# Optimization experiments

Hardware: AMD Instinct MI355X
Metric: run time of the kernel (lower is better)

The kernel has to match this reference:

```python
import jax, jax.numpy as jnp
import numpy as np
import math

NUM_HEADS = 16
KEY_SIZE = 64
HIDDEN = 4096
EMBED = 1024
VOCAB = 32000
SEQ = 2048
LAYERS = 4


def rmsnorm(x):
    return x * jax.lax.rsqrt(jnp.mean(x * x, axis=-1, keepdims=True) + 1e-5)


def rope_buffers(seq, d):
    half = d // 2
    i = jnp.arange(d)
    offset = i % half
    scales = jnp.power(10000.0, (-2.0 / d) * offset.astype(jnp.float32))
    m = jnp.arange(seq, dtype=jnp.float32)
    angles = m[:, None] * scales[None, :]  # [S, D]
    cos = jnp.cos(angles)
    sin = jnp.sin(angles)
    sin = jnp.concatenate([-sin[:, :half], sin[:, half:]], axis=-1)
    return cos, sin


def rotate(x, cos, sin):
    # x: [B, H, S, D]; cos/sin: [S, D]
    half = KEY_SIZE // 2
    swapped = jnp.concatenate([x[..., half:], x[..., :half]], axis=-1)
    return cos[None, None] * x + sin[None, None] * swapped


def setup_inputs() -> dict:
    key = jax.random.key(0)
    ks = jax.random.split(key, 7)
    std = 0.02
    return {
        'tokens': jax.random.randint(ks[0], (1, SEQ), 0, VOCAB),
        'table': jax.random.normal(ks[1], (VOCAB, EMBED), jnp.float32) * std,
        'qkv_w': jax.random.normal(ks[2], (LAYERS, EMBED, 3 * NUM_HEADS * KEY_SIZE), jnp.float32) * std,
        'out_w': jax.random.normal(ks[3], (LAYERS, NUM_HEADS * KEY_SIZE, EMBED), jnp.float32) * std,
        'up_w': jax.random.normal(ks[4], (LAYERS, EMBED, 2 * HIDDEN), jnp.float32) * std,
        'down_w': jax.random.normal(ks[5], (LAYERS, HIDDEN, EMBED), jnp.float32) * std,
        'vocab_w': jax.random.normal(ks[6], (EMBED, VOCAB), jnp.float32) * std,
    }


def reference(tokens, table, qkv_w, out_w, up_w, down_w, vocab_w):
    B, S = tokens.shape
    H, D = NUM_HEADS, KEY_SIZE
    # module zeroes embedding row 0 each forward
    table = table.at[0].set(0.0)
    cos, sin = rope_buffers(S, D)
    causal = jnp.tril(jnp.ones((S, S), dtype=bool))  # context_size == S -> pure causal
    emb = table[tokens]  # [B, S, E]
    for l in range(LAYERS):
        # --- self attention ---
        normed = rmsnorm(emb)
        qkv = normed @ qkv_w[l]  # [B, S, 3HD]
        q, k, v = jnp.split(qkv, 3, axis=-1)
        q = q.reshape(B, S, H, D).transpose(0, 2, 1, 3)
        k = k.reshape(B, S, H, D).transpose(0, 2, 1, 3)
        v = v.reshape(B, S, H, D).transpose(0, 2, 1, 3)
        q = rotate(q, cos, sin)
        k = rotate(k, cos, sin)
        attn = jnp.einsum('bhqd,bhkd->bhqk', q, k) / math.sqrt(D)
        attn = jnp.where(causal[None, None], attn, -jnp.inf)
        attn = jax.nn.softmax(attn, axis=-1)
        out = jnp.einsum('bhqk,bhkd->bhqd', attn, v)
        out = out.transpose(0, 2, 1, 3).reshape(B, S, H * D)
        emb = emb + out @ out_w[l]
        # --- SwiGLU FFN ---
        normed = rmsnorm(emb)
        gate_up = normed @ up_w[l]
        gate, up = gate_up[..., :HIDDEN], gate_up[..., HIDDEN:]
        emb = emb + (up * jax.nn.silu(gate)) @ down_w[l]
    emb = rmsnorm(emb)
    logits = emb @ vocab_w  # [B, S, V]
    return logits
```

## Files before the change

kernel.cpp:

```cpp
#include <hip/hip_runtime.h>
#include <hip/hip_bf16.h>

typedef __attribute__((ext_vector_type(8))) short short8;
typedef __attribute__((ext_vector_type(4))) float f32x4;

__device__ __forceinline__ ushort f2bf(float f) {
  uint32_t u = __float_as_uint(f);
  uint32_t r = (u + 0x7FFFu + ((u >> 16) & 1u)) >> 16;
  return (ushort)r;
}
__device__ __forceinline__ float bf2f(ushort u) {
  return __uint_as_float(((uint32_t)u) << 16);
}

__device__ __forceinline__ void gload_lds16(const ushort* g, ushort* l) {
  __builtin_amdgcn_global_load_lds(
      (const __attribute__((address_space(1))) void*)g,
      (__attribute__((address_space(3))) void*)l, 16, 0, 0);
}

__device__ __forceinline__ f32x4 mfma16(short8 a, short8 b, f32x4 c) {
  return __builtin_amdgcn_mfma_f32_16x16x32_bf16(a, b, c, 0, 0, 0);
}

#define BAR() __builtin_amdgcn_s_barrier()
#define WAIT_LGKM()                                        \
  do {                                                     \
    asm volatile("s_waitcnt lgkmcnt(0)" ::: "memory");     \
    __builtin_amdgcn_sched_barrier(0);                     \
  } while (0)
#define WAIT_VM0()                                         \
  do {                                                     \
    asm volatile("s_waitcnt vmcnt(0)" ::: "memory");       \
    __builtin_amdgcn_sched_barrier(0);                     \
  } while (0)
#define WAIT_VM4()                                         \
  do {                                                     \
    asm volatile("s_waitcnt vmcnt(4)" ::: "memory");       \
    __builtin_amdgcn_sched_barrier(0);                     \
  } while (0)

__global__ __launch_bounds__(256)
void transpose_conv_kernel(const float* __restrict__ W, ushort* __restrict__ WT,
                           const int K, const int N, const int mode) {
  const size_t lofs = (size_t)blockIdx.z * K * N;
  W += lofs;
  WT += lofs;
  __shared__ float tile[64][65];
  const int n0 = blockIdx.x * 64;
  const int k0 = blockIdx.y * 64;
  const int t = threadIdx.x;
#pragma unroll
  for (int j = 0; j < 4; ++j) {
    const int idx = j * 1024 + t * 4;
    const int kk = idx >> 6, nn = idx & 63;
    *(float4*)&tile[kk][nn] = *(const float4*)&W[(size_t)(k0 + kk) * N + n0 + nn];
  }
  __syncthreads();
#pragma unroll
  for (int j = 0; j < 4; ++j) {
    const int idx = j * 1024 + t * 4;
    const int nn = idx >> 6, kk = idx & 63;
    int rr = n0 + nn;
    if (mode == 1) rr = (rr < 4096) ? (2 * rr) : (2 * (rr - 4096) + 1);
    ushort4 o;
    o.x = f2bf(tile[kk + 0][nn]);
    o.y = f2bf(tile[kk + 1][nn]);
    o.z = f2bf(tile[kk + 2][nn]);
    o.w = f2bf(tile[kk + 3][nn]);
    *(ushort4*)&WT[(size_t)rr * K + k0 + kk] = o;
  }
}

__global__ __launch_bounds__(256)
void sincos_kernel(float2* __restrict__ cstab) {
  const int idx = blockIdx.x * 256 + threadIdx.x;
  const int s = idx >> 5, o = idx & 31;
  const float freq = exp2f(-0.41524101186092029f * (float)o);
  const float a = (float)s * freq;
  cstab[idx] = make_float2(cosf(a), sinf(a));
}

__global__ __launch_bounds__(256)
void embed_norm_kernel(const int* __restrict__ tokens, const float* __restrict__ table,
                       float* __restrict__ emb, ushort* __restrict__ normed) {
  const int s = blockIdx.x, t = threadIdx.x;
  const int tok = tokens[s];
  float4 v = make_float4(0.f, 0.f, 0.f, 0.f);
  if (tok != 0) v = *(const float4*)&table[(size_t)tok * 1024 + t * 4];
  *(float4*)&emb[(size_t)s * 1024 + t * 4] = v;
  float ss = v.x * v.x + v.y * v.y + v.z * v.z + v.w * v.w;
#pragma unroll
  for (int off = 32; off; off >>= 1) ss += __shfl_xor(ss, off);
  __shared__ float red[4];
  if ((t & 63) == 0) red[t >> 6] = ss;
  __syncthreads();
  const float total = red[0] + red[1] + red[2] + red[3];
  const float sc = rsqrtf(total * (1.f / 1024.f) + 1e-5f);
  ushort4 o;
  o.x = f2bf(v.x * sc); o.y = f2bf(v.y * sc);
  o.z = f2bf(v.z * sc); o.w = f2bf(v.w * sc);
  *(ushort4*)&normed[(size_t)s * 1024 + t * 4] = o;
}

__global__ __launch_bounds__(256)
void rmsnorm_kernel(const float* __restrict__ x, ushort* __restrict__ out) {
  const int row = blockIdx.x, t = threadIdx.x;
  const float4 v = *(const float4*)&x[(size_t)row * 1024 + t * 4];
  float ss = v.x * v.x + v.y * v.y + v.z * v.z + v.w * v.w;
#pragma unroll
  for (int off = 32; off; off >>= 1) ss += __shfl_xor(ss, off);
  __shared__ float red[4];
  if ((t & 63) == 0) red[t >> 6] = ss;
  __syncthreads();
  const float total = red[0] + red[1] + red[2] + red[3];
  const float sc = rsqrtf(total * (1.f / 1024.f) + 1e-5f);
  ushort4 o;
  o.x = f2bf(v.x * sc); o.y = f2bf(v.y * sc);
  o.z = f2bf(v.z * sc); o.w = f2bf(v.w * sc);
  *(ushort4*)&out[(size_t)row * 1024 + t * 4] = o;
}

__global__ __launch_bounds__(512)
void attn_mfma_kernel(const ushort* __restrict__ qh, const ushort* __restrict__ kh,
                      const ushort* __restrict__ vt, float* __restrict__ wso,
                      float* __restrict__ wsml) {
  __shared__ ushort sQ[128 * 64];
  __shared__ ushort sK[2][64 * 64];
  __shared__ ushort sV[2][64 * 64];
  __shared__ ushort sP[8][1024];
  const int h = blockIdx.y;
  const int u = blockIdx.x;
  const int qt_raw = u >> 1, half = u & 1;
  const int qt = (h < 8) ? qt_raw : 15 - qt_raw;
  const int i0 = qt * 128;
  const int tid = threadIdx.x;
  const int w = tid >> 6, lane = tid & 63;
  const int llo = lane & 15, lhi = lane >> 4;
  const ushort* qg = qh + ((size_t)h * 2048 + i0) * 64;
  const ushort* kg = kh + (size_t)h * 2048 * 64;
  const ushort* vg = vt + (size_t)h * 64 * 2048;

  const int scb = w * 64;
  const int sch = scb + lane;
  const int srow = sch >> 3, sc = sch & 7;
  auto stage_kv = [&](int kb, int b) {
    gload_lds16(kg + (size_t)(kb + srow) * 64 + ((sc ^ (srow & 7)) * 8),
                &sK[b][scb * 8]);
    gload_lds16(vg + (size_t)srow * 2048 + kb + ((sc ^ (srow & 7)) * 8),
                &sV[b][scb * 8]);
  };

  const int c0 = half ? (qt + 1) : 0;
  const int c1 = half ? (2 * qt + 2) : (qt + 1);

#pragma unroll
  for (int j = 0; j < 2; ++j) {
    const int cb = j * 512 + w * 64;
    const int ch = cb + lane;
    const int row = ch >> 3, c = ch & 7;
    gload_lds16(qg + (size_t)row * 64 + ((c ^ (row & 7)) * 8), &sQ[cb * 8]);
  }
  stage_kv(c0 * 64, 0);
  __syncthreads();
  const int qrow = w * 16 + llo;
  const short8 qf0 = *(const short8*)&sQ[qrow * 64 + ((lhi ^ (qrow & 7)) * 8)];
  const short8 qf1 = *(const short8*)&sQ[qrow * 64 + (((4 + lhi) ^ (qrow & 7)) * 8)];
  const int wmax = i0 + w * 16 + 15;

  float m = -1e30f, lsum = 0.f;
  f32x4 o[4] = {};
  int bufc = 0;
  for (int cb2 = c0; cb2 < c1; ++cb2) {
    const int kb = cb2 * 64;
    if (cb2 + 1 < c1) stage_kv((cb2 + 1) * 64, bufc ^ 1);

    if (kb <= wmax) {
      f32x4 st[4] = {};
#pragma unroll
      for (int ck = 0; ck < 2; ++ck) {
        const short8 qf = ck ? qf1 : qf0;
#pragma unroll
        for (int f = 0; f < 4; ++f) {
          const int key = f * 16 + llo;
          const short8 kf = *(const short8*)&sK[bufc][key * 64 + (((ck * 4 + lhi) ^ (key & 7)) * 8)];
          st[f] = mfma16(kf, qf, st[f]);
        }
      }

      float pv[4][4];
      const bool edge = (kb + 63 > i0 + w * 16);
#pragma unroll
      for (int f = 0; f < 4; ++f)
#pragma unroll
        for (int r = 0; r < 4; ++r) {
          float x = st[f][r] * 0.125f;
          if (edge && (kb - i0 + f * 16 + lhi * 4 + r) > qrow) x = -1e30f;
          pv[f][r] = x;
        }
      float mr = pv[0][0];
#pragma unroll
      for (int f = 0; f < 4; ++f)
#pragma unroll
        for (int r = 0; r < 4; ++r) mr = fmaxf(mr, pv[f][r]);
      mr = fmaxf(mr, __shfl_xor(mr, 16));
      mr = fmaxf(mr, __shfl_xor(mr, 32));
      const float mnew = fmaxf(m, mr);
      const float scale = __expf(m - mnew);
      m = mnew;
      float rs = 0.f;
#pragma unroll
      for (int f = 0; f < 4; ++f)
#pragma unroll
        for (int r = 0; r < 4; ++r) {
          const float p = __expf(pv[f][r] - mnew);
          pv[f][r] = p;
          rs += p;
        }
      rs += __shfl_xor(rs, 16);
      rs += __shfl_xor(rs, 32);
      lsum = lsum * scale + rs;
      float scr[4];
#pragma unroll
      for (int r = 0; r < 4; ++r) scr[r] = __shfl(scale, lhi * 4 + r);
#pragma unroll
      for (int nn = 0; nn < 4; ++nn)
#pragma unroll
        for (int r = 0; r < 4; ++r) o[nn][r] *= scr[r];

      ushort* pw = sP[w];
#pragma unroll
      for (int f = 0; f < 4; ++f) {
        uint2 pk;
        pk.x = (uint)f2bf(pv[f][0]) | ((uint)f2bf(pv[f][1]) << 16);
        pk.y = (uint)f2bf(pv[f][2]) | ((uint)f2bf(pv[f][3]) << 16);
        *(uint2*)&pw[llo * 64 + ((f * 16 + lhi * 4) ^ ((llo & 7) << 3))] = pk;
      }
      const short8 pf0 = *(const short8*)&pw[llo * 64 + ((lhi ^ (llo & 7)) * 8)];
      const short8 pf1 = *(const short8*)&pw[llo * 64 + (((4 + lhi) ^ (llo & 7)) * 8)];

#pragma unroll
      for (int ck = 0; ck < 2; ++ck) {
        const short8 pf = ck ? pf1 : pf0;
#pragma unroll
        for (int nn = 0; nn < 4; ++nn) {
          const int drow = nn * 16 + llo;
          const short8 vf = *(const short8*)&sV[bufc][drow * 64 + (((ck * 4 + lhi) ^ (drow & 7)) * 8)];
          o[nn] = mfma16(pf, vf, o[nn]);
        }
      }
    }

    __syncthreads();
    bufc ^= 1;
  }

#pragma unroll
  for (int nn = 0; nn < 4; ++nn)
#pragma unroll
    for (int r = 0; r < 4; ++r) {
      const int row = i0 + w * 16 + lhi * 4 + r;
      wso[((size_t)(half * 16 + h) * 2048 + row) * 64 + nn * 16 + llo] = o[nn][r];
    }
  if (lhi == 0) {
    const int row = i0 + w * 16 + llo;
    *(float2*)&wsml[((size_t)(half * 16 + h) * 2048 + row) * 2] = make_float2(m, lsum);
  }
}

__global__ __launch_bounds__(256)
void attn_merge_kernel(const float* __restrict__ wso, const float* __restrict__ wsml,
                       ushort* __restrict__ attn_out) {
  const int row = blockIdx.x;
  const int t = threadIdx.x;
  const int h = t >> 4, dg = t & 15;
  const float2 ml1 = *(const float2*)&wsml[((size_t)h * 2048 + row) * 2];
  const float2 ml2 = *(const float2*)&wsml[((size_t)(16 + h) * 2048 + row) * 2];
  const float m = fmaxf(ml1.x, ml2.x);
  const float w1 = __expf(ml1.x - m), w2 = __expf(ml2.x - m);
  const float inv = 1.f / (ml1.y * w1 + ml2.y * w2);
  const float4 o1 = *(const float4*)&wso[((size_t)h * 2048 + row) * 64 + dg * 4];
  const float4 o2 = *(const float4*)&wso[((size_t)(16 + h) * 2048 + row) * 64 + dg * 4];
  ushort4 o;
  o.x = f2bf((o1.x * w1 + o2.x * w2) * inv);
  o.y = f2bf((o1.y * w1 + o2.y * w2) * inv);
  o.z = f2bf((o1.z * w1 + o2.z * w2) * inv);
  o.w = f2bf((o1.w * w1 + o2.w * w2) * inv);
  *(ushort4*)&attn_out[(size_t)row * 1024 + h * 64 + dg * 4] = o;
}

template <int BM, int BN, int EPI>
__global__ __launch_bounds__(256)
void gemm_bt64_kernel(const ushort* __restrict__ A, const ushort* __restrict__ BT,
                      const float* __restrict__ addend, void* __restrict__ Cout,
                      const int M, const int N, const int K) {
  constexpr int WM = BM / 2, WN = BN / 2;
  constexpr int FM = WM / 16, FN = WN / 16;
  __shared__ ushort sA[BM * 64];
  __shared__ ushort sB[BN * 64];
  const int bm0 = blockIdx.y * BM;
  const int bn0 = blockIdx.x * BN;
  const int tid = threadIdx.x;
  const int wid = tid >> 6, lane = tid & 63;
  const int wr = wid >> 1, wc = wid & 1;
  const int lhi = lane >> 4, llo = lane & 15;
  f32x4 acc[FM][FN] = {};
  for (int kt = 0; kt < K; kt += 64) {
#pragma unroll
    for (int i = 0; i < BM * 8 / 256; ++i) {
      const int cb = i * 256 + wid * 64;
      const int ch = cb + lane;
      const int row = ch >> 3, c = ch & 7;
      gload_lds16(A + (size_t)(bm0 + row) * K + kt + ((c ^ (row & 7)) * 8),
                  sA + (size_t)cb * 8);
    }
#pragma unroll
    for (int i = 0; i < BN * 8 / 256; ++i) {
      const int cb = i * 256 + wid * 64;
      const int ch = cb + lane;
      const int row = ch >> 3, c = ch & 7;
      gload_lds16(BT + (size_t)(bn0 + row) * K + kt + ((c ^ (row & 7)) * 8),
                  sB + (size_t)cb * 8);
    }
    __syncthreads();
    short8 aF[FM][2], bF[FN][2];
#pragma unroll
    for (int mm = 0; mm < FM; ++mm) {
      const int row = wr * WM + mm * 16 + llo;
#pragma unroll
      for (int ks = 0; ks < 2; ++ks)
        aF[mm][ks] = *(const short8*)&sA[row * 64 + (((ks * 4 + lhi) ^ (row & 7)) * 8)];
    }
#pragma unroll
    for (int nn = 0; nn < FN; ++nn) {
      const int row = wc * WN + nn * 16 + llo;
#pragma unroll
      for (int ks = 0; ks < 2; ++ks)
        bF[nn][ks] = *(const short8*)&sB[row * 64 + (((ks * 4 + lhi) ^ (row & 7)) * 8)];
    }
#pragma unroll
    for (int mm = 0; mm < FM; ++mm)
#pragma unroll
      for (int nn = 0; nn < FN; ++nn)
#pragma unroll
        for (int ks = 0; ks < 2; ++ks)
          acc[mm][nn] = mfma16(aF[mm][ks], bF[nn][ks], acc[mm][nn]);
    __syncthreads();
  }
#pragma unroll
  for (int mm = 0; mm < FM; ++mm) {
#pragma unroll
    for (int nn = 0; nn < FN; ++nn) {
      const int col = bn0 + wc * WN + nn * 16 + llo;
#pragma unroll
      for (int r = 0; r < 4; ++r) {
        const int row = bm0 + wr * WM + mm * 16 + lhi * 4 + r;
        float v = acc[mm][nn][r];
        if constexpr (EPI == 1) v += addend[(size_t)row * N + col];
        ((float*)Cout)[(size_t)row * N + col] = v;
      }
    }
  }
}

__global__ __launch_bounds__(256)
void gemm_qkv_kernel(const ushort* __restrict__ A, const ushort* __restrict__ BT,
                     const float2* __restrict__ cstab, ushort* __restrict__ qh,
                     ushort* __restrict__ kh, ushort* __restrict__ vt, const int K) {
  constexpr int BM = 128, BN = 128, WM = 64, WN = 64, FM = 4, FN = 4;
  __shared__ ushort sA[BM * 64];
  __shared__ ushort sB[BN * 64];
  const int bm0 = blockIdx.y * BM;
  const int bn0 = blockIdx.x * BN;
  const int tid = threadIdx.x;
  const int wid = tid >> 6, lane = tid & 63;
  const int wr = wid >> 1, wc = wid & 1;
  const int lhi = lane >> 4, llo = lane & 15;
  f32x4 acc[FM][FN] = {};
  for (int kt = 0; kt < K; kt += 64) {
#pragma unroll
    for (int i = 0; i < 4; ++i) {
      const int cb = i * 256 + wid * 64;
      const int ch = cb + lane;
      const int row = ch >> 3, c = ch & 7;
      gload_lds16(A + (size_t)(bm0 + row) * K + kt + ((c ^ (row & 7)) * 8),
                  sA + (size_t)cb * 8);
    }
#pragma unroll
    for (int i = 0; i < 4; ++i) {
      const int cb = i * 256 + wid * 64;
      const int ch = cb + lane;
      const int row = ch >> 3, c = ch & 7;
      gload_lds16(BT + (size_t)(bn0 + row) * K + kt + ((c ^ (row & 7)) * 8),
                  sB + (size_t)cb * 8);
    }
    __syncthreads();
    short8 aF[FM][2], bF[FN][2];
#pragma unroll
    for (int mm = 0; mm < FM; ++mm) {
      const int row = wr * WM + mm * 16 + llo;
#pragma unroll
      for (int ks = 0; ks < 2; ++ks)
        aF[mm][ks] = *(const short8*)&sA[row * 64 + (((ks * 4 + lhi) ^ (row & 7)) * 8)];
    }
#pragma unroll
    for (int nn = 0; nn < FN; ++nn) {
      const int row = wc * WN + nn * 16 + llo;
#pragma unroll
      for (int ks = 0; ks < 2; ++ks)
        bF[nn][ks] = *(const short8*)&sB[row * 64 + (((ks * 4 + lhi) ^ (row & 7)) * 8)];
    }
#pragma unroll
    for (int mm = 0; mm < FM; ++mm)
#pragma unroll
      for (int nn = 0; nn < FN; ++nn)
#pragma unroll
        for (int ks = 0; ks < 2; ++ks)
          acc[mm][nn] = mfma16(aF[mm][ks], bF[nn][ks], acc[mm][nn]);
    __syncthreads();
  }
#pragma unroll
  for (int mm = 0; mm < FM; ++mm) {
    const int row_base = bm0 + wr * WM + mm * 16 + lhi * 4;
#pragma unroll
    for (int nn = 0; nn < FN; ++nn) {
      const int col = bn0 + wc * WN + nn * 16 + llo;
      const int part = col >> 10;
      const int hcol = col & 1023;
      const int h = hcol >> 6;
      const int d = hcol & 63;
      const int off = d & 31;
      if (part == 2) {
        ushort4 o;
        o.x = f2bf(acc[mm][nn][0]);
        o.y = f2bf(acc[mm][nn][1]);
        o.z = f2bf(acc[mm][nn][2]);
        o.w = f2bf(acc[mm][nn][3]);
        *(ushort4*)&vt[((size_t)h * 64 + d) * 2048 + row_base] = o;
      } else {
#pragma unroll
        for (int r = 0; r < 4; ++r) {
          const int row = row_base + r;
          const float v = acc[mm][nn][r];
          const float pt = acc[mm][nn ^ 2][r];
          const float2 cn = cstab[row * 32 + off];
          const float si = (d < 32) ? -cn.y : cn.y;
          const ushort o = f2bf(cn.x * v + si * pt);
          const size_t ho = ((size_t)h * 2048 + row) * 64 + d;
          if (part == 0) qh[ho] = o; else kh[ho] = o;
        }
      }
    }
  }
}

template <int EPI>
__global__ __launch_bounds__(512, 2)
void gemm8p_kernel(const ushort* __restrict__ A, const ushort* __restrict__ BT,
                   void* __restrict__ Cout,
                   const int M, const int N, const int K, const int nby) {
  extern __shared__ ushort smem[];
  const int nwg = gridDim.x;
  const int cpx = nwg >> 3;
  int id = blockIdx.x;
  id = (id & 7) * cpx + (id >> 3);
  const int by = id % nby, bx = id / nby;
  const int bm0 = by * 256, bn0 = bx * 256;
  const int tid = threadIdx.x;
  const int wid = tid >> 6, lane = tid & 63;
  const int wr = wid >> 2, wc = wid & 3;
  const int llo = lane & 15, lhi = lane >> 4;
  const ushort* gA = A + (size_t)bm0 * K;
  const ushort* gB = BT + (size_t)bn0 * K;

  auto stage = [&](ushort* dst, int kt) {
#pragma unroll
    for (int i = 0; i < 2; ++i) {
      const int cb = i * 512 + wid * 64;
      const int ch = cb + lane;
      const int row = ch >> 2, c = ch & 3;
      gload_lds16(gA + (size_t)row * K + kt + ((c ^ ((row >> 1) & 3)) * 8),
                  dst + (size_t)cb * 8);
    }
#pragma unroll
    for (int i = 0; i < 2; ++i) {
      const int cb = i * 512 + wid * 64;
      const int ch = cb + lane;
      const int row = ch >> 2, c = ch & 3;
      gload_lds16(gB + (size_t)row * K + kt + ((c ^ ((row >> 1) & 3)) * 8),
                  dst + 8192 + (size_t)cb * 8);
    }
  };

  f32x4 acc[8][4] = {};
  short8 aF[4], bF[4];

  const int nt = K >> 5;
  stage(smem, 0);
  stage(smem + 16384, 32);
  WAIT_VM4();
  BAR();

  int cs = 0;
  for (int t = 0; t < nt; ++t) {
    ushort* cA = smem + cs * 16384;
    ushort* cB = cA + 8192;
    int ss = cs + 2; if (ss >= 3) ss -= 3;
    const bool pf2 = (t + 2 < nt);
    if (pf2) stage(smem + ss * 16384, (t + 2) * 32);
#pragma unroll
    for (int mm = 0; mm < 4; ++mm) {
      const int row = wr * 128 + mm * 16 + llo;
      aF[mm] = *(const short8*)&cA[row * 32 + ((lhi ^ ((row >> 1) & 3)) * 8)];
    }
#pragma unroll
    for (int nn = 0; nn < 4; ++nn) {
      const int row = wc * 64 + nn * 16 + llo;
      bF[nn] = *(const short8*)&cB[row * 32 + ((lhi ^ ((row >> 1) & 3)) * 8)];
    }
    BAR(); WAIT_LGKM();
    __builtin_amdgcn_s_setprio(1);
#pragma unroll
    for (int mm = 0; mm < 4; ++mm)
#pragma unroll
      for (int nn = 0; nn < 4; ++nn)
        acc[mm][nn] = mfma16(aF[mm], bF[nn], acc[mm][nn]);
    __builtin_amdgcn_s_setprio(0);
    BAR();
#pragma unroll
    for (int mm = 0; mm < 4; ++mm) {
      const int row = wr * 128 + (mm + 4) * 16 + llo;
      aF[mm] = *(const short8*)&cA[row * 32 + ((lhi ^ ((row >> 1) & 3)) * 8)];
    }
    BAR(); WAIT_LGKM();
    __builtin_amdgcn_s_setprio(1);
#pragma unroll
    for (int mm = 0; mm < 4; ++mm)
#pragma unroll
      for (int nn = 0; nn < 4; ++nn)
        acc[mm + 4][nn] = mfma16(aF[mm], bF[nn], acc[mm + 4][nn]);
    __builtin_amdgcn_s_setprio(0);
    if (pf2) { WAIT_VM4(); } else { WAIT_VM0(); }
    BAR();
    ++cs; if (cs == 3) cs = 0;
  }

#pragma unroll
  for (int m = 0; m < 8; ++m) {
#pragma unroll
    for (int n = 0; n < 4; ++n) {
      const int col = bn0 + wc * 64 + n * 16 + llo;
#pragma unroll
      for (int r = 0; r < 4; ++r) {
        const int row = bm0 + wr * 128 + m * 16 + lhi * 4 + r;
        float v = acc[m][n][r];
        if constexpr (EPI == 3) {
          const float other = __shfl_xor(v, 1);
          if ((llo & 1) == 0) {
            const float gate = v, up = other;
            const float hh = up * gate / (1.f + expf(-gate));
            ((ushort*)Cout)[(size_t)row * (N >> 1) + (col >> 1)] = f2bf(hh);
          }
        } else {
          ((float*)Cout)[(size_t)row * N + col] = v;
        }
      }
    }
  }
}

extern "C" void kernel_launch(void* const* d_in, const int* in_sizes, int n_in,
                              void* d_out, int out_size, void* d_ws, size_t ws_size,
                              hipStream_t stream) {
  const int* tokens    = (const int*)d_in[0];
  const float* table   = (const float*)d_in[1];
  const float* qkv_w   = (const float*)d_in[2];
  const float* out_w   = (const float*)d_in[3];
  const float* up_w    = (const float*)d_in[4];
  const float* down_w  = (const float*)d_in[5];
  const float* vocab_w = (const float*)d_in[6];
  float* logits = (float*)d_out;

  constexpr int G8P_LDS = 98304;
  hipFuncSetAttribute(reinterpret_cast<const void*>(&gemm8p_kernel<0>),
                      hipFuncAttributeMaxDynamicSharedMemorySize, G8P_LDS);
  hipFuncSetAttribute(reinterpret_cast<const void*>(&gemm8p_kernel<3>),
                      hipFuncAttributeMaxDynamicSharedMemorySize, G8P_LDS);

  char* p = (char*)d_ws;
  auto alloc = [&](size_t bytes) {
    char* r = p;
    p += (bytes + 255) & ~(size_t)255;
    return r;
  };
  float*  emb    = (float*)alloc(2048ull * 1024 * 4);
  ushort* normed = (ushort*)alloc(2048ull * 1024 * 2);
  float2* cstab  = (float2*)alloc(2048ull * 32 * 8);
  ushort* qhb    = (ushort*)alloc(16ull * 2048 * 64 * 2);
  ushort* khb    = (ushort*)alloc(16ull * 2048 * 64 * 2);
  ushort* vtb    = (ushort*)alloc(16ull * 64 * 2048 * 2);
  ushort* attno  = (ushort*)alloc(2048ull * 1024 * 2);
  float*  wso    = (float*)alloc(2ull * 16 * 2048 * 64 * 4);
  float*  wsml   = (float*)alloc(2ull * 16 * 2048 * 2 * 4);
  ushort* hbuf   = (ushort*)alloc(2048ull * 4096 * 2);
  ushort* qkvT   = (ushort*)alloc(4ull * 3072 * 1024 * 2);
  ushort* outT   = (ushort*)alloc(4ull * 1024 * 1024 * 2);
  ushort* upT    = (ushort*)alloc(4ull * 8192 * 1024 * 2);
  ushort* downT  = (ushort*)alloc(4ull * 1024 * 4096 * 2);
  ushort* vocabT = (ushort*)alloc(32000ull * 1024 * 2);

  transpose_conv_kernel<<<dim3(3072 / 64, 1024 / 64, 4), 256, 0, stream>>>(
      qkv_w, qkvT, 1024, 3072, 0);
  transpose_conv_kernel<<<dim3(1024 / 64, 1024 / 64, 4), 256, 0, stream>>>(
      out_w, outT, 1024, 1024, 0);
  transpose_conv_kernel<<<dim3(8192 / 64, 1024 / 64, 4), 256, 0, stream>>>(
      up_w, upT, 1024, 8192, 1);
  transpose_conv_kernel<<<dim3(1024 / 64, 4096 / 64, 4), 256, 0, stream>>>(
      down_w, downT, 4096, 1024, 0);
  transpose_conv_kernel<<<dim3(32000 / 64, 1024 / 64, 1), 256, 0, stream>>>(
      vocab_w, vocabT, 1024, 32000, 0);
  sincos_kernel<<<256, 256, 0, stream>>>(cstab);

  embed_norm_kernel<<<2048, 256, 0, stream>>>(tokens, table, emb, normed);

  for (int l = 0; l < 4; ++l) {
    if (l > 0) rmsnorm_kernel<<<2048, 256, 0, stream>>>(emb, normed);
    gemm_qkv_kernel<<<dim3(3072 / 128, 2048 / 128), 256, 0, stream>>>(
        normed, qkvT + (size_t)l * 3072 * 1024, cstab, qhb, khb, vtb, 1024);
    attn_mfma_kernel<<<dim3(32, 16), 512, 0, stream>>>(qhb, khb, vtb, wso, wsml);
    attn_merge_kernel<<<2048, 256, 0, stream>>>(wso, wsml, attno);
    gemm_bt64_kernel<64, 128, 1><<<dim3(1024 / 128, 2048 / 64), 256, 0, stream>>>(
        attno, outT + (size_t)l * 1024 * 1024, emb, emb, 2048, 1024, 1024);
    rmsnorm_kernel<<<2048, 256, 0, stream>>>(emb, normed);
    gemm8p_kernel<3><<<(8192 / 256) * (2048 / 256), 512, G8P_LDS, stream>>>(
        normed, upT + (size_t)l * 8192 * 1024, hbuf, 2048, 8192, 1024, 2048 / 256);
    gemm_bt64_kernel<64, 128, 1><<<dim3(1024 / 128, 2048 / 64), 256, 0, stream>>>(
        hbuf, downT + (size_t)l * 1024 * 4096, emb, emb, 2048, 1024, 4096);
  }
  rmsnorm_kernel<<<2048, 256, 0, stream>>>(emb, normed);
  gemm8p_kernel<0><<<(32000 / 256) * (2048 / 256), 512, G8P_LDS, stream>>>(
      normed, vocabT, logits, 2048, 32000, 1024, 2048 / 256);
}
```

Measured before the change: 1.191 ms.

## Double-buffer LDS tiles in GEMM kernels to overlap loads with MFMA

```diff
diff --git a/kernel.cpp b/kernel.cpp
--- a/kernel.cpp
+++ b/kernel.cpp
@@ -296,23 +296,23 @@
                       const int M, const int N, const int K) {
   constexpr int WM = BM / 2, WN = BN / 2;
   constexpr int FM = WM / 16, FN = WN / 16;
-  __shared__ ushort sA[BM * 64];
-  __shared__ ushort sB[BN * 64];
+  __shared__ ushort sA[2][BM * 64];
+  __shared__ ushort sB[2][BN * 64];
   const int bm0 = blockIdx.y * BM;
   const int bn0 = blockIdx.x * BN;
   const int tid = threadIdx.x;
   const int wid = tid >> 6, lane = tid & 63;
   const int wr = wid >> 1, wc = wid & 1;
   const int lhi = lane >> 4, llo = lane & 15;
-  f32x4 acc[FM][FN] = {};
-  for (int kt = 0; kt < K; kt += 64) {
+
+  auto stage = [&](int kt, int b) {
 #pragma unroll
     for (int i = 0; i < BM * 8 / 256; ++i) {
       const int cb = i * 256 + wid * 64;
       const int ch = cb + lane;
       const int row = ch >> 3, c = ch & 7;
       gload_lds16(A + (size_t)(bm0 + row) * K + kt + ((c ^ (row & 7)) * 8),
-                  sA + (size_t)cb * 8);
+                  &sA[b][(size_t)cb * 8]);
     }
 #pragma unroll
     for (int i = 0; i < BN * 8 / 256; ++i) {
@@ -320,23 +320,31 @@
       const int ch = cb + lane;
       const int row = ch >> 3, c = ch & 7;
       gload_lds16(BT + (size_t)(bn0 + row) * K + kt + ((c ^ (row & 7)) * 8),
-                  sB + (size_t)cb * 8);
-    }
-    __syncthreads();
+                  &sB[b][(size_t)cb * 8]);
+    }
+  };
+
+  f32x4 acc[FM][FN] = {};
+  const int nt = K >> 6;
+  stage(0, 0);
+  __syncthreads();
+  int buf = 0;
+  for (int t = 0; t < nt; ++t) {
+    if (t + 1 < nt) stage((t + 1) * 64, buf ^ 1);
     short8 aF[FM][2], bF[FN][2];
 #pragma unroll
     for (int mm = 0; mm < FM; ++mm) {
       const int row = wr * WM + mm * 16 + llo;
 #pragma unroll
       for (int ks = 0; ks < 2; ++ks)
-        aF[mm][ks] = *(const short8*)&sA[row * 64 + (((ks * 4 + lhi) ^ (row & 7)) * 8)];
+        aF[mm][ks] = *(const short8*)&sA[buf][row * 64 + (((ks * 4 + lhi) ^ (row & 7)) * 8)];
     }
 #pragma unroll
     for (int nn = 0; nn < FN; ++nn) {
       const int row = wc * WN + nn * 16 + llo;
 #pragma unroll
       for (int ks = 0; ks < 2; ++ks)
-        bF[nn][ks] = *(const short8*)&sB[row * 64 + (((ks * 4 + lhi) ^ (row & 7)) * 8)];
+        bF[nn][ks] = *(const short8*)&sB[buf][row * 64 + (((ks * 4 + lhi) ^ (row & 7)) * 8)];
     }
 #pragma unroll
     for (int mm = 0; mm < FM; ++mm)
@@ -346,6 +354,7 @@
         for (int ks = 0; ks < 2; ++ks)
           acc[mm][nn] = mfma16(aF[mm][ks], bF[nn][ks], acc[mm][nn]);
     __syncthreads();
+    buf ^= 1;
   }
 #pragma unroll
   for (int mm = 0; mm < FM; ++mm) {
@@ -368,23 +377,23 @@
                      const float2* __restrict__ cstab, ushort* __restrict__ qh,
                      ushort* __restrict__ kh, ushort* __restrict__ vt, const int K) {
   constexpr int BM = 128, BN = 128, WM = 64, WN = 64, FM = 4, FN = 4;
-  __shared__ ushort sA[BM * 64];
-  __shared__ ushort sB[BN * 64];
+  __shared__ ushort sA[2][BM * 64];
+  __shared__ ushort sB[2][BN * 64];
   const int bm0 = blockIdx.y * BM;
   const int bn0 = blockIdx.x * BN;
   const int tid = threadIdx.x;
   const int wid = tid >> 6, lane = tid & 63;
   const int wr = wid >> 1, wc = wid & 1;
   const int lhi = lane >> 4, llo = lane & 15;
-  f32x4 acc[FM][FN] = {};
-  for (int kt = 0; kt < K; kt += 64) {
+
+  auto stage = [&](int kt, int b) {
 #pragma unroll
     for (int i = 0; i < 4; ++i) {
       const int cb = i * 256 + wid * 64;
       const int ch = cb + lane;
       const int row = ch >> 3, c = ch & 7;
       gload_lds16(A + (size_t)(bm0 + row) * K + kt + ((c ^ (row & 7)) * 8),
-                  sA + (size_t)cb * 8);
+                  &sA[b][(size_t)cb * 8]);
     }
 #pragma unroll
     for (int i = 0; i < 4; ++i) {
@@ -392,23 +401,31 @@
       const int ch = cb + lane;
       const int row = ch >> 3, c = ch & 7;
       gload_lds16(BT + (size_t)(bn0 + row) * K + kt + ((c ^ (row & 7)) * 8),
-                  sB + (size_t)cb * 8);
-    }
-    __syncthreads();
+                  &sB[b][(size_t)cb * 8]);
+    }
+  };
+
+  f32x4 acc[FM][FN] = {};
+  const int nt = K >> 6;
+  stage(0, 0);
+  __syncthreads();
+  int buf = 0;
+  for (int t = 0; t < nt; ++t) {
+    if (t + 1 < nt) stage((t + 1) * 64, buf ^ 1);
     short8 aF[FM][2], bF[FN][2];
 #pragma unroll
     for (int mm = 0; mm < FM; ++mm) {
       const int row = wr * WM + mm * 16 + llo;
 #pragma unroll
       for (int ks = 0; ks < 2; ++ks)
-        aF[mm][ks] = *(const short8*)&sA[row * 64 + (((ks * 4 + lhi) ^ (row & 7)) * 8)];
+        aF[mm][ks] = *(const short8*)&sA[buf][row * 64 + (((ks * 4 + lhi) ^ (row & 7)) * 8)];
     }
 #pragma unroll
     for (int nn = 0; nn < FN; ++nn) {
       const int row = wc * WN + nn * 16 + llo;
 #pragma unroll
       for (int ks = 0; ks < 2; ++ks)
-        bF[nn][ks] = *(const short8*)&sB[row * 64 + (((ks * 4 + lhi) ^ (row & 7)) * 8)];
+        bF[nn][ks] = *(const short8*)&sB[buf][row * 64 + (((ks * 4 + lhi) ^ (row & 7)) * 8)];
     }
 #pragma unroll
     for (int mm = 0; mm < FM; ++mm)
@@ -418,6 +435,7 @@
         for (int ks = 0; ks < 2; ++ks)
           acc[mm][nn] = mfma16(aF[mm][ks], bF[nn][ks], acc[mm][nn]);
     __syncthreads();
+    buf ^= 1;
   }
 #pragma unroll
   for (int mm = 0; mm < FM; ++mm) {
```

Result: faster. 1.161 ms (-2.6%).
